# Optimization experiments

Hardware: AMD Instinct MI355X
Metric: run time of the kernel (lower is better)

The kernel has to match this reference:

```python
import jax, jax.numpy as jnp
import numpy as np

BLOCK = 64  # bitsandbytes 4-bit blocksize
OUT, IN = 4096, 4096
# NF4 codebook (bitsandbytes values)
NF4_CODE = np.array([
    -1.0, -0.6961928009986877, -0.5250730514526367, -0.39491748809814453,
    -0.28444138169288635, -0.18477343022823334, -0.09105003625154495, 0.0,
    0.07958029955625534, 0.16093020141124725, 0.24611230194568634,
    0.33791524171829224, 0.44070982933044434, 0.5626170039176941,
    0.7229568362236023, 1.0], dtype=np.float32)


def setup_inputs() -> dict:
    key = jax.random.key(0)
    k1, k2, k3 = jax.random.split(key, 3)
    x = jax.random.normal(k1, (8, 2048, IN), dtype=jnp.float32)
    qweight = jax.random.randint(k2, (OUT * IN,), 0, 16, dtype=jnp.int32)
    absmax = jax.random.uniform(k3, (OUT * IN // BLOCK,), dtype=jnp.float32)
    return {"x": x, "qweight": qweight, "absmax": absmax}


def reference(x, qweight, absmax):
    code = jnp.asarray(NF4_CODE)
    # dequantize: codebook lookup, then per-block absmax scaling
    w = code[qweight].reshape(-1, BLOCK) * absmax[:, None]  # [n_blocks, BLOCK]
    W = w.reshape(OUT, IN)                                   # [out, in]
    # linear: y = x @ W^T  (no bias: quantized_bias is None)
    return jnp.einsum('bsi,oi->bso', x, W)
```

## Files before the change

kernel.cpp:

```cpp
#include <hip/hip_runtime.h>
#include <hip/hip_bf16.h>
#include <stdint.h>

#define IN_DIM  4096
#define OUT_DIM 4096
#define M_DIM   16384
#define BK      64
#define NT      (IN_DIM / BK)

typedef float f32x4 __attribute__((ext_vector_type(4)));
typedef short bf16x8 __attribute__((ext_vector_type(8)));
typedef short bf16x4 __attribute__((ext_vector_type(4)));
typedef int   i32x4 __attribute__((ext_vector_type(4)));

__device__ __constant__ float NF4_CODE_D[16] = {
    -1.0f, -0.6961928009986877f, -0.5250730514526367f, -0.39491748809814453f,
    -0.28444138169288635f, -0.18477343022823334f, -0.09105003625154495f, 0.0f,
    0.07958029955625534f, 0.16093020141124725f, 0.24611230194568634f,
    0.33791524171829224f, 0.44070982933044434f, 0.5626170039176941f,
    0.7229568362236023f, 1.0f};

static __device__ __forceinline__ ushort f2bf(float f) {
  union { float f; uint32_t u; } v; v.f = f;
  uint32_t r = v.u + 0x7FFFu + ((v.u >> 16) & 1u);
  return (ushort)(r >> 16);
}

#define NB_W 8192
__global__ void prep(const float* __restrict__ x, const int* __restrict__ q,
                     const float* __restrict__ am, ushort* __restrict__ xb,
                     ushort* __restrict__ w) {
  if (blockIdx.x < NB_W) {
    __shared__ float code[16];
    if (threadIdx.x < 16) code[threadIdx.x] = NF4_CODE_D[threadIdx.x];
    __syncthreads();
    size_t t = (size_t)blockIdx.x * 256 + threadIdx.x;
    size_t base = t * 8;
    i32x4 qa = *(const i32x4*)(q + base);
    i32x4 qb = *(const i32x4*)(q + base + 4);
    float s = am[base >> 6];
    bf16x8 o;
    o[0] = (short)f2bf(code[qa[0] & 15] * s);
    o[1] = (short)f2bf(code[qa[1] & 15] * s);
    o[2] = (short)f2bf(code[qa[2] & 15] * s);
    o[3] = (short)f2bf(code[qa[3] & 15] * s);
    o[4] = (short)f2bf(code[qb[0] & 15] * s);
    o[5] = (short)f2bf(code[qb[1] & 15] * s);
    o[6] = (short)f2bf(code[qb[2] & 15] * s);
    o[7] = (short)f2bf(code[qb[3] & 15] * s);
    *(bf16x8*)(w + base) = o;
  } else {
    size_t t = (size_t)(blockIdx.x - NB_W) * 256 + threadIdx.x;
    size_t base = t * 8;
    f32x4 a = *(const f32x4*)(x + base);
    f32x4 b = *(const f32x4*)(x + base + 4);
    bf16x8 o;
    o[0] = (short)f2bf(a[0]); o[1] = (short)f2bf(a[1]);
    o[2] = (short)f2bf(a[2]); o[3] = (short)f2bf(a[3]);
    o[4] = (short)f2bf(b[0]); o[5] = (short)f2bf(b[1]);
    o[6] = (short)f2bf(b[2]); o[7] = (short)f2bf(b[3]);
    *(bf16x8*)(xb + base) = o;
  }
}

static __device__ __forceinline__ void llds16(const ushort* g, ushort* l) {
  __builtin_amdgcn_global_load_lds(
      (const __attribute__((address_space(1))) void*)g,
      (__attribute__((address_space(3))) void*)l, 16, 0, 0);
}

__global__ __launch_bounds__(512, 2) void gemm256(const ushort* __restrict__ Xb,
                                                  const ushort* __restrict__ W,
                                                  float* __restrict__ Y) {
  __shared__ ushort As[2][256 * BK];
  __shared__ ushort Bs[2][256 * BK];

  const int tid  = threadIdx.x;
  const int lane = tid & 63;
  const int wid  = tid >> 6;
  const int wr   = wid >> 2;
  const int wc   = wid & 3;
  const int l15  = lane & 15;
  const int kg   = lane >> 4;
  const int l7   = lane & 7;

  const int bid = blockIdx.x;
  const int wg  = (bid & 7) * 128 + (bid >> 3);
  const int tm  = wg >> 4;
  const int tn  = wg & 15;
  const size_t row0 = (size_t)tm * 256;
  const size_t col0 = (size_t)tn * 256;

  const int srow  = tid >> 3;
  const int scol8 = ((tid & 7) ^ (srow & 7)) * 8;
  const int wbase = wid << 9;

  f32x4  acc[8][4] = {};
  bf16x8 aA[4][2], aB[4][2], b0[2][2], b1[2][2];

#define BARX()   asm volatile("s_barrier" ::: "memory")
#define LGKM0()  do { asm volatile("s_waitcnt lgkmcnt(0)" ::: "memory"); \
                      __builtin_amdgcn_sched_barrier(0); } while (0)
#define LGKM8()  asm volatile("s_waitcnt lgkmcnt(8)" ::: "memory")
#define VMC(n)   asm volatile("s_waitcnt vmcnt(" #n ")" ::: "memory")
#define PRI1()   __builtin_amdgcn_s_setprio(1)
#define PRI0()   __builtin_amdgcn_s_setprio(0)

#define STAGE_A(kt, h, nb) do { \
    llds16(Xb + (row0 + (h)*128 +  0 + srow) * IN_DIM + (kt)*BK + scol8, \
           &As[nb][(h)*8192 +    0 + wbase]); \
    llds16(Xb + (row0 + (h)*128 + 64 + srow) * IN_DIM + (kt)*BK + scol8, \
           &As[nb][(h)*8192 + 4096 + wbase]); \
  } while (0)

#define STAGE_B(kt, h, nb) do { \
    llds16(W + (col0 + (h)*128 +  0 + srow) * IN_DIM + (kt)*BK + scol8, \
           &Bs[nb][(h)*8192 +    0 + wbase]); \
    llds16(W + (col0 + (h)*128 + 64 + srow) * IN_DIM + (kt)*BK + scol8, \
           &Bs[nb][(h)*8192 + 4096 + wbase]); \
  } while (0)

#define LDA_(dst, nb, mh) do { \
    _Pragma("unroll") for (int mi = 0; mi < 4; ++mi) \
    _Pragma("unroll") for (int ks = 0; ks < 2; ++ks) \
      dst[mi][ks] = *(const bf16x8*)&As[nb][((mh)*128 + wr*64 + mi*16 + l15) * BK \
                                            + (((ks*4 + kg) ^ l7) * 8)]; \
  } while (0)

#define LDB_(dst, nb, nh) do { \
    _Pragma("unroll") for (int ni = 0; ni < 2; ++ni) \
    _Pragma("unroll") for (int ks = 0; ks < 2; ++ks) \
      dst[ni][ks] = *(const bf16x8*)&Bs[nb][((nh)*128 + wc*32 + ni*16 + l15) * BK \
                                            + (((ks*4 + kg) ^ l7) * 8)]; \
  } while (0)

#define QUAD(mh, nh, aR, bR) do { PRI1(); \
    _Pragma("unroll") for (int mi = 0; mi < 4; ++mi) \
    _Pragma("unroll") for (int ni = 0; ni < 2; ++ni) \
    _Pragma("unroll") for (int ks = 0; ks < 2; ++ks) \
      acc[(mh)*4 + mi][(nh)*2 + ni] = __builtin_amdgcn_mfma_f32_16x16x32_bf16( \
          aR[mi][ks], bR[ni][ks], acc[(mh)*4 + mi][(nh)*2 + ni], 0, 0, 0); \
    PRI0(); } while (0)

  STAGE_A(0, 0, 0); STAGE_B(0, 0, 0); STAGE_A(0, 1, 0); STAGE_B(0, 1, 0);
  STAGE_A(1, 0, 1); STAGE_B(1, 0, 1); STAGE_A(1, 1, 1);
  VMC(6); BARX();

#pragma unroll 1
  for (int t = 0; t < NT - 2; ++t) {
    const int cur = t & 1, nxt = cur ^ 1;
    LDA_(aA, cur, 0); LDB_(b0, cur, 0);
    STAGE_B(t + 1, 1, nxt);
    LGKM8();
    BARX(); LGKM0();
    QUAD(0, 0, aA, b0);
    BARX();
    LDB_(b1, cur, 1);
    STAGE_A(t + 2, 0, cur);
    BARX(); LGKM0();
    QUAD(0, 1, aA, b1);
    BARX();
    LDA_(aB, cur, 1);
    STAGE_B(t + 2, 0, cur);
    BARX(); LGKM0();
    QUAD(1, 0, aB, b0);
    BARX();
    STAGE_A(t + 2, 1, cur);
    VMC(6);
    BARX();
    QUAD(1, 1, aB, b1);
    BARX();
  }

  LDA_(aA, 0, 0); LDB_(b0, 0, 0);
  STAGE_B(NT - 1, 1, 1);
  LGKM8();
  BARX(); LGKM0();
  QUAD(0, 0, aA, b0);
  BARX();
  LDB_(b1, 0, 1);
  BARX(); LGKM0();
  QUAD(0, 1, aA, b1);
  BARX();
  LDA_(aB, 0, 1);
  BARX(); LGKM0();
  QUAD(1, 0, aB, b0);
  BARX();
  VMC(0);
  BARX();
  QUAD(1, 1, aB, b1);
  BARX();

  LDA_(aA, 1, 0); LDB_(b0, 1, 0);
  QUAD(0, 0, aA, b0);
  LDB_(b1, 1, 1);
  QUAD(0, 1, aA, b1);
  LDA_(aB, 1, 1);
  QUAD(1, 0, aB, b0);
  QUAD(1, 1, aB, b1);

#undef QUAD
#undef LDB_
#undef LDA_
#undef STAGE_B
#undef STAGE_A

  float* yb = Y + (row0 + wr * 64 + kg * 4) * OUT_DIM + col0 + wc * 32 + l15;
#pragma unroll
  for (int mh = 0; mh < 2; ++mh)
#pragma unroll
    for (int mi = 0; mi < 4; ++mi)
#pragma unroll
      for (int nh = 0; nh < 2; ++nh)
#pragma unroll
        for (int ni = 0; ni < 2; ++ni)
#pragma unroll
          for (int v = 0; v < 4; ++v)
            yb[(size_t)(mh * 128 + mi * 16 + v) * OUT_DIM + nh * 128 + ni * 16] =
                acc[mh * 4 + mi][nh * 2 + ni][v];
}

__global__ void gemm_fb(const float* __restrict__ X, const ushort* __restrict__ W,
                        float* __restrict__ Y) {
  __shared__ ushort Af[128 * 64];
  __shared__ ushort Bf[128 * 64];
  const int tid  = threadIdx.x;
  const int lane = tid & 63;
  const int wid  = tid >> 6;
  const int wr   = wid >> 1, wc = wid & 1;
  const int bid  = blockIdx.x;
  const int tm   = bid / 32, tn = bid % 32;
  const size_t row0 = (size_t)tm * 128, col0 = (size_t)tn * 128;
  f32x4 acc[4][4] = {};
  const int arow = lane & 15, kgrp = lane >> 4;
  const int srow = lane >> 3, scol = (lane & 7) * 8;
  for (int k0 = 0; k0 < IN_DIM; k0 += 64) {
    f32x4 r[8];
#pragma unroll
    for (int i = 0; i < 8; ++i)
      r[i] = *(const f32x4*)(X + (row0 + i * 16 + (tid >> 4)) * IN_DIM + k0 + (tid & 15) * 4);
#pragma unroll
    for (int i = 0; i < 8; ++i) {
      bf16x4 o;
      o[0] = (short)f2bf(r[i][0]); o[1] = (short)f2bf(r[i][1]);
      o[2] = (short)f2bf(r[i][2]); o[3] = (short)f2bf(r[i][3]);
      *(bf16x4*)&Af[(i * 16 + (tid >> 4)) * 64 + (tid & 15) * 4] = o;
    }
#pragma unroll
    for (int i = 0; i < 4; ++i) {
      const int c = wid * 4 + i;
      llds16(W + (col0 + c * 8 + srow) * IN_DIM + k0 + scol, Bf + c * 512);
    }
    __syncthreads();
#pragma unroll
    for (int ks = 0; ks < 2; ++ks) {
      bf16x8 a[4], b[4];
#pragma unroll
      for (int m = 0; m < 4; ++m)
        a[m] = *(const bf16x8*)&Af[(wr * 64 + m * 16 + arow) * 64 + ks * 32 + kgrp * 8];
#pragma unroll
      for (int n = 0; n < 4; ++n)
        b[n] = *(const bf16x8*)&Bf[(wc * 64 + n * 16 + arow) * 64 + ks * 32 + kgrp * 8];
#pragma unroll
      for (int m = 0; m < 4; ++m)
#pragma unroll
        for (int n = 0; n < 4; ++n)
          acc[m][n] = __builtin_amdgcn_mfma_f32_16x16x32_bf16(a[m], b[n], acc[m][n], 0, 0, 0);
    }
    __syncthreads();
  }
  float* yb = Y + (row0 + wr * 64) * OUT_DIM + col0 + wc * 64;
  const int crow = (lane >> 4) * 4, ccol = lane & 15;
#pragma unroll
  for (int m = 0; m < 4; ++m)
#pragma unroll
    for (int n = 0; n < 4; ++n)
#pragma unroll
      for (int v = 0; v < 4; ++v)
        yb[(size_t)(m * 16 + crow + v) * OUT_DIM + n * 16 + ccol] = acc[m][n][v];
}

extern "C" void kernel_launch(void* const* d_in, const int* in_sizes, int n_in,
                              void* d_out, int out_size, void* d_ws, size_t ws_size,
                              hipStream_t stream) {
  const float* x  = (const float*)d_in[0];
  const int*   q  = (const int*)d_in[1];
  const float* am = (const float*)d_in[2];
  float* y = (float*)d_out;

  ushort* w = (ushort*)d_ws;
  const size_t WB = (size_t)OUT_DIM * IN_DIM * sizeof(ushort);
  const size_t XB = (size_t)M_DIM * IN_DIM * sizeof(ushort);

  if (ws_size >= WB + XB) {
    ushort* xb = (ushort*)((char*)d_ws + WB);
    const int nb = NB_W + (int)((size_t)M_DIM * IN_DIM / 8 / 256);
    prep<<<nb, 256, 0, stream>>>(x, q, am, xb, w);
    gemm256<<<(M_DIM / 256) * (OUT_DIM / 256), 512, 0, stream>>>(xb, w, y);
  } else {
    prep<<<NB_W, 256, 0, stream>>>(x, q, am, nullptr, w);
    gemm_fb<<<(M_DIM / 128) * (OUT_DIM / 128), 256, 0, stream>>>(x, w, y);
  }
}
```

Baseline: 694.2 us.

## Replace fine-grained ping-pong schedule with simple double-buffered prefetch loop

The interleaved schedule is replaced by a plain double-buffered main loop. Each iteration issues every global-to-LDS load for the next K tile up front, waits on the vmcnt and one barrier, runs all four MFMA quadrants, and ends with a single barrier. This drops the s_setprio priority hints, the explicit lgkmcnt waits and most of the per-quadrant barriers, and shortens the prologue and epilogue. The aim is to cut synchronisation overhead. The cost is coarser overlap between memory staging and MFMA work, plus a hazard of stalls on LDS reads that the compiler now has to schedule on its own.

```diff
diff --git a/kernel.cpp b/kernel.cpp
--- a/kernel.cpp
+++ b/kernel.cpp
@@ -98,13 +98,8 @@
   f32x4  acc[8][4] = {};
   bf16x8 aA[4][2], aB[4][2], b0[2][2], b1[2][2];
 
-#define BARX()   asm volatile("s_barrier" ::: "memory")
-#define LGKM0()  do { asm volatile("s_waitcnt lgkmcnt(0)" ::: "memory"); \
-                      __builtin_amdgcn_sched_barrier(0); } while (0)
-#define LGKM8()  asm volatile("s_waitcnt lgkmcnt(8)" ::: "memory")
-#define VMC(n)   asm volatile("s_waitcnt vmcnt(" #n ")" ::: "memory")
-#define PRI1()   __builtin_amdgcn_s_setprio(1)
-#define PRI0()   __builtin_amdgcn_s_setprio(0)
+#define BARX()  asm volatile("s_barrier" ::: "memory")
+#define VMC(n)  asm volatile("s_waitcnt vmcnt(" #n ")" ::: "memory")
 
 #define STAGE_A(kt, h, nb) do { \
     llds16(Xb + (row0 + (h)*128 +  0 + srow) * IN_DIM + (kt)*BK + scol8, \
@@ -134,70 +129,42 @@
                                             + (((ks*4 + kg) ^ l7) * 8)]; \
   } while (0)
 
-#define QUAD(mh, nh, aR, bR) do { PRI1(); \
+#define QUAD(mh, nh, aR, bR) do { \
     _Pragma("unroll") for (int mi = 0; mi < 4; ++mi) \
     _Pragma("unroll") for (int ni = 0; ni < 2; ++ni) \
     _Pragma("unroll") for (int ks = 0; ks < 2; ++ks) \
       acc[(mh)*4 + mi][(nh)*2 + ni] = __builtin_amdgcn_mfma_f32_16x16x32_bf16( \
           aR[mi][ks], bR[ni][ks], acc[(mh)*4 + mi][(nh)*2 + ni], 0, 0, 0); \
-    PRI0(); } while (0)
+  } while (0)
 
   STAGE_A(0, 0, 0); STAGE_B(0, 0, 0); STAGE_A(0, 1, 0); STAGE_B(0, 1, 0);
-  STAGE_A(1, 0, 1); STAGE_B(1, 0, 1); STAGE_A(1, 1, 1);
-  VMC(6); BARX();
 
 #pragma unroll 1
-  for (int t = 0; t < NT - 2; ++t) {
+  for (int t = 0; t < NT - 1; ++t) {
     const int cur = t & 1, nxt = cur ^ 1;
+    STAGE_A(t + 1, 0, nxt); STAGE_B(t + 1, 0, nxt);
+    STAGE_A(t + 1, 1, nxt); STAGE_B(t + 1, 1, nxt);
+    VMC(8);
+    BARX();
     LDA_(aA, cur, 0); LDB_(b0, cur, 0);
-    STAGE_B(t + 1, 1, nxt);
-    LGKM8();
-    BARX(); LGKM0();
     QUAD(0, 0, aA, b0);
-    BARX();
     LDB_(b1, cur, 1);
-    STAGE_A(t + 2, 0, cur);
-    BARX(); LGKM0();
     QUAD(0, 1, aA, b1);
-    BARX();
     LDA_(aB, cur, 1);
-    STAGE_B(t + 2, 0, cur);
-    BARX(); LGKM0();
+    QUAD(1, 1, aB, b1);
     QUAD(1, 0, aB, b0);
     BARX();
-    STAGE_A(t + 2, 1, cur);
-    VMC(6);
-    BARX();
-    QUAD(1, 1, aB, b1);
-    BARX();
-  }
-
-  LDA_(aA, 0, 0); LDB_(b0, 0, 0);
-  STAGE_B(NT - 1, 1, 1);
-  LGKM8();
-  BARX(); LGKM0();
-  QUAD(0, 0, aA, b0);
-  BARX();
-  LDB_(b1, 0, 1);
-  BARX(); LGKM0();
-  QUAD(0, 1, aA, b1);
-  BARX();
-  LDA_(aB, 0, 1);
-  BARX(); LGKM0();
-  QUAD(1, 0, aB, b0);
-  BARX();
+  }
+
   VMC(0);
   BARX();
-  QUAD(1, 1, aB, b1);
-  BARX();
-
   LDA_(aA, 1, 0); LDB_(b0, 1, 0);
   QUAD(0, 0, aA, b0);
   LDB_(b1, 1, 1);
   QUAD(0, 1, aA, b1);
   LDA_(aB, 1, 1);
+  QUAD(1, 1, aB, b1);
   QUAD(1, 0, aB, b0);
-  QUAD(1, 1, aB, b1);
 
 #undef QUAD
 #undef LDB_
```

New measurement: 701.2 us. Within noise of the previous version (+1.0%).
